# Performance work log

Measured on AMD Instinct MI355X. Metric: run time of the kernel, lower is better.

Reference implementation:

```python
import jax, jax.numpy as jnp
import numpy as np

DIM = 512
NUM_HEADS = 8
HEAD_SIZE = 64
INNER = NUM_HEADS * HEAD_SIZE  # 512


def setup_inputs() -> dict:
    key = jax.random.key(0)
    k1, k2, k3, k4, k5 = jax.random.split(key, 5)
    x = jax.random.normal(k1, (2, 4096, DIM), dtype=jnp.float32)
    # Linear params stored as [in, out] for y = x @ W + b (same math as torch Linear)
    w_qkv = jax.random.normal(k2, (DIM, INNER * 3), dtype=jnp.float32) * (1.0 / np.sqrt(DIM))
    b_qkv = jax.random.normal(k3, (INNER * 3,), dtype=jnp.float32) * 0.01
    w_out = jax.random.normal(k4, (INNER, DIM), dtype=jnp.float32) * (1.0 / np.sqrt(INNER))
    b_out = jax.random.normal(k5, (DIM,), dtype=jnp.float32) * 0.01
    return {"x": x, "w_qkv": w_qkv, "b_qkv": b_qkv, "w_out": w_out, "b_out": b_out}


def reference(x, w_qkv, b_qkv, w_out, b_out):
    b, n, _ = x.shape
    qkv = x @ w_qkv + b_qkv                      # [b, n, 3*inner]
    q, k, v = jnp.split(qkv, 3, axis=-1)          # each [b, n, inner]

    def heads(t):  # 'b n (h d) -> b h n d'
        return t.reshape(b, n, NUM_HEADS, HEAD_SIZE).transpose(0, 2, 1, 3)

    q, k, v = heads(q), heads(k), heads(v)
    scores = jnp.einsum('bhnd,bhmd->bhnm', q, k) / jnp.sqrt(jnp.float32(HEAD_SIZE))
    probs = jax.nn.softmax(scores, axis=-1)       # dropout is identity in eval
    out = jnp.einsum('bhnm,bhmd->bhnd', probs, v)
    out = out.transpose(0, 2, 1, 3).reshape(b, n, INNER)  # 'b h n d -> b n (h d)'
    return out @ w_out + b_out
```

## Files before the change

kernel.cpp:

```cpp
#include <hip/hip_runtime.h>

typedef __bf16 bf16;
typedef __bf16 bf16x8 __attribute__((ext_vector_type(8)));
typedef float f32x4 __attribute__((ext_vector_type(4)));
typedef unsigned u32x4 __attribute__((ext_vector_type(4)));

#define MFMA16(a, b, c) __builtin_amdgcn_mfma_f32_16x16x32_bf16((a), (b), (c), 0, 0, 0)

static __device__ __forceinline__ bf16x8 ldg8(const bf16* p) {
  return *(const bf16x8*)p;
}
static __device__ __forceinline__ unsigned cvt_pk_bf16(float lo, float hi) {
  unsigned d;
  asm("v_cvt_pk_bf16_f32 %0, %1, %2" : "=v"(d) : "v"(lo), "v"(hi));
  return d;
}
static __device__ __forceinline__ void pl32_swap(unsigned& a, unsigned& b) {
  asm("v_permlane32_swap_b32 %0, %1" : "+v"(a), "+v"(b));
}
static __device__ __forceinline__ void pl16_swap(unsigned& a, unsigned& b) {
  asm("v_permlane16_swap_b32 %0, %1" : "+v"(a), "+v"(b));
}


__global__ __launch_bounds__(256) void prep(const float* __restrict__ Wqkv,
                                            const float* __restrict__ Wout,
                                            const float* __restrict__ x,
                                            bf16* __restrict__ Wp1,
                                            bf16* __restrict__ Wp2,
                                            bf16* __restrict__ Xp) {
  __shared__ float tile[32 * 129];
  if (blockIdx.x < 16) {
    int kc = blockIdx.x, nt = blockIdx.y;
    const float* W;
    bf16* dst;
    int N, ntl;
    if (nt < 12) {
      W = Wqkv; N = 1536; ntl = nt;
      dst = Wp1 + ((size_t)ntl * 16 + kc) * 4096;
    } else {
      W = Wout; N = 512; ntl = nt - 12;
      dst = Wp2 + ((size_t)ntl * 16 + kc) * 4096;
    }
    int row = threadIdx.x >> 3;
    int c0 = (threadIdx.x & 7) * 16;
    const float* src = W + (size_t)(kc * 32 + row) * N + ntl * 128 + c0;
#pragma unroll
    for (int i = 0; i < 4; i++) {
      float4 v = *(const float4*)(src + i * 4);
      tile[row * 129 + c0 + i * 4 + 0] = v.x;
      tile[row * 129 + c0 + i * 4 + 1] = v.y;
      tile[row * 129 + c0 + i * 4 + 2] = v.z;
      tile[row * 129 + c0 + i * 4 + 3] = v.w;
    }
    __syncthreads();
#pragma unroll
    for (int half = 0; half < 2; half++) {
      int U = threadIdx.x + half * 256;
      int kchunk = U >> 7, n = U & 127;
      bf16x8 o;
#pragma unroll
      for (int j = 0; j < 8; j++) o[j] = (bf16)tile[(kchunk * 8 + j) * 129 + n];
      *(bf16x8*)&dst[U * 8] = o;
    }
  } else {
    int mt = blockIdx.x - 16, kc = blockIdx.y;
    int r = threadIdx.x >> 1;
    int khalf = threadIdx.x & 1;
    const float* src = x + (size_t)(mt * 128 + r) * 512 + kc * 32 + khalf * 16;
    float4 v0 = *(const float4*)(src + 0);
    float4 v1 = *(const float4*)(src + 4);
    float4 v2 = *(const float4*)(src + 8);
    float4 v3 = *(const float4*)(src + 12);
    bf16* dt = Xp + ((size_t)mt * 16 + kc) * 4096;
    bf16x8 a, b;
    a[0] = (bf16)v0.x; a[1] = (bf16)v0.y; a[2] = (bf16)v0.z; a[3] = (bf16)v0.w;
    a[4] = (bf16)v1.x; a[5] = (bf16)v1.y; a[6] = (bf16)v1.z; a[7] = (bf16)v1.w;
    b[0] = (bf16)v2.x; b[1] = (bf16)v2.y; b[2] = (bf16)v2.z; b[3] = (bf16)v2.w;
    b[4] = (bf16)v3.x; b[5] = (bf16)v3.y; b[6] = (bf16)v3.z; b[7] = (bf16)v3.w;
    int kc0 = khalf * 2;
    *(bf16x8*)&dt[(kc0 + 0) * 1024 + r * 8] = a;
    *(bf16x8*)&dt[(kc0 + 1) * 1024 + r * 8] = b;
  }
}

__global__ __launch_bounds__(256, 3) void qkv_gemm(const bf16* __restrict__ Xp,
                                                   const bf16* __restrict__ Wp1,
                                                   const float* __restrict__ bqkv,
                                                   bf16* __restrict__ Q,
                                                   bf16* __restrict__ Kh,
                                                   bf16* __restrict__ Vt) {
  int mt = blockIdx.x, nt = blockIdx.y;
  int tid = threadIdx.x;
  int wave = tid >> 6, lane = tid & 63;
  int l16 = lane & 15, quad = lane >> 4;
  int wr = wave >> 1, wc = wave & 1;

  __shared__ __align__(16) bf16 SM[9216];

  const bf16* At = Xp + (size_t)mt * 16 * 4096;
  const bf16* Bt = Wp1 + (size_t)nt * 16 * 4096;

  bf16x8 pa0 = ldg8(At + tid * 8);
  bf16x8 pa1 = ldg8(At + 2048 + tid * 8);

  f32x4 acc[4][4] = {};
#pragma unroll 2
  for (int kc = 0; kc < 16; kc++) {
    bf16* A = SM + (kc & 1) * 4096;
    *(bf16x8*)&A[tid * 8] = pa0;
    *(bf16x8*)&A[2048 + tid * 8] = pa1;
    __syncthreads();
    if (kc < 15) {
      const bf16* an = At + (kc + 1) * 4096;
      pa0 = ldg8(an + tid * 8);
      pa1 = ldg8(an + 2048 + tid * 8);
    }
    bf16x8 af[4], bfr[4];
#pragma unroll
    for (int fi = 0; fi < 4; fi++)
      af[fi] = *(const bf16x8*)&A[(quad * 128 + wr * 64 + fi * 16 + l16) * 8];
    const bf16* Bk = Bt + kc * 4096;
#pragma unroll
    for (int fj = 0; fj < 4; fj++)
      bfr[fj] = ldg8(Bk + (quad * 128 + wc * 64 + fj * 16 + l16) * 8);
    __builtin_amdgcn_s_setprio(1);
#pragma unroll
    for (int fi = 0; fi < 4; fi++)
#pragma unroll
      for (int fj = 0; fj < 4; fj++)
        acc[fi][fj] = MFMA16(af[fi], bfr[fj], acc[fi][fj]);
    __builtin_amdgcn_s_setprio(0);
  }

  __syncthreads();
  const int TS = 72;
  int b = mt >> 5;

  if (nt < 8) {
    bool isQ = nt < 4;
    bf16* dstb = isQ ? Q : Kh;
    int hb = isQ ? nt * 2 : (nt - 4) * 2;
#pragma unroll
    for (int ph = 0; ph < 2; ph++) {
      if (wc == ph) {
#pragma unroll
        for (int fj = 0; fj < 4; fj++) {
          float bias = bqkv[nt * 128 + wc * 64 + fj * 16 + l16];
#pragma unroll
          for (int fi = 0; fi < 4; fi++)
#pragma unroll
            for (int rr = 0; rr < 4; rr++) {
              float v = acc[fi][fj][rr] + bias;
              if (isQ) v *= 0.18033688f;
              SM[(wr * 64 + fi * 16 + quad * 4 + rr) * TS + fj * 16 + l16] =
                  (bf16)v;
            }
        }
      }
      __syncthreads();
      int bh = b * 8 + hb + ph;
      bf16* dh = dstb + (size_t)bh * 4096 * 64 + (size_t)((mt & 31) * 128) * 64;
#pragma unroll
      for (int i = 0; i < 4; i++) {
        int U = tid + i * 256;
        int mr = U >> 3, oct = U & 7;
        bf16x8 v = ldg8(&SM[mr * TS + oct * 8]);
        *(bf16x8*)&dh[(size_t)mr * 64 + oct * 8] = v;
      }
      __syncthreads();
    }
  } else {
    int h0 = (nt - 8) * 2;
#pragma unroll
    for (int ph = 0; ph < 2; ph++) {
      if (wr == ph) {
#pragma unroll
        for (int fj = 0; fj < 4; fj++) {
          float bias = bqkv[nt * 128 + wc * 64 + fj * 16 + l16];
          int cp = wc * 64 + fj * 16 + l16;
#pragma unroll
          for (int fi = 0; fi < 4; fi++)
#pragma unroll
            for (int rr = 0; rr < 4; rr++)
              SM[cp * TS + fi * 16 + quad * 4 + rr] =
                  (bf16)(acc[fi][fj][rr] + bias);
        }
      }
      __syncthreads();
      int nb = (mt & 31) * 2 + ph;
#pragma unroll
      for (int i = 0; i < 4; i++) {
        int U = tid + i * 256;
        int cp = U >> 3, oct = U & 7;
        int h = h0 + (cp >> 6), d = cp & 63;
        int bh = b * 8 + h;
        bf16x8 v = ldg8(&SM[cp * TS + oct * 8]);
        *(bf16x8*)&Vt[(((size_t)bh * 64 + nb) * 64 + d) * 64 + oct * 8] = v;
      }
      __syncthreads();
    }
  }
}

__global__ __launch_bounds__(256, 4) void flash_partial(const bf16* __restrict__ Q,
                                                        const bf16* __restrict__ K,
                                                        const bf16* __restrict__ Vt,
                                                        bf16* __restrict__ Opart,
                                                        float* __restrict__ Lpart) {
  int i = blockIdx.x;
  int swz = (i & 7) * 128 + (i >> 3);
  int half = swz & 1;
  int strip = (swz >> 1) & 31;
  int bh = swz >> 6;
  int tid = threadIdx.x;
  int wave = tid >> 6, lane = tid & 63;
  int l16 = lane & 15, quad = lane >> 4;

  const bf16* Qh = Q + (size_t)bh * 4096 * 64;
  const bf16* Kg = K + ((size_t)bh * 4096 + half * 2048) * 64;
  const bf16* Vg = Vt + (size_t)bh * 64 * 4096 + (size_t)half * 2048 * 64;

  __shared__ __align__(16) bf16 Klds[2][4096];
  __shared__ __align__(16) bf16 Vlds[2][4096];

  int qbase = strip * 128 + wave * 32;
  bf16x8 aq[2][2];
#pragma unroll
  for (int mt = 0; mt < 2; mt++) {
    const bf16* qr = Qh + (size_t)(qbase + mt * 16 + l16) * 64;
    aq[mt][0] = ldg8(qr + quad * 8);
    aq[mt][1] = ldg8(qr + 32 + quad * 8);
  }

  bf16x8 ones;
#pragma unroll
  for (int j = 0; j < 8; j++) ones[j] = (bf16)1.0f;

  f32x4 o[2][4] = {};
  f32x4 acc_l[2] = {};

  int e0 = tid * 8, e1 = (256 + tid) * 8;
  int r0 = e0 >> 6, r1 = e1 >> 6;
  int u0 = r0 * 8 + (((e0 & 63) >> 3) ^ (r0 & 7));
  int u1 = r1 * 8 + (((e1 & 63) >> 3) ^ (r1 & 7));

  bf16x8 kp0 = ldg8(Kg + e0), kp1 = ldg8(Kg + e1);
  bf16x8 vp0 = ldg8(Vg + e0), vp1 = ldg8(Vg + e1);

#pragma unroll 2
  for (int t = 0; t < 32; t++) {
    int cur = t & 1;
    bf16* kl = Klds[cur];
    bf16* vl = Vlds[cur];
    *(bf16x8*)&kl[u0 * 8] = kp0;
    *(bf16x8*)&kl[u1 * 8] = kp1;
    *(bf16x8*)&vl[u0 * 8] = vp0;
    *(bf16x8*)&vl[u1 * 8] = vp1;
    __syncthreads();

    if (t < 31) {
      const bf16* kg = Kg + (size_t)(t + 1) * 4096;
      const bf16* vg = Vg + (size_t)(t + 1) * 4096;
      kp0 = ldg8(kg + e0);
      kp1 = ldg8(kg + e1);
      vp0 = ldg8(vg + e0);
      vp1 = ldg8(vg + e1);
    }

#pragma unroll
    for (int h2 = 0; h2 < 2; h2++) {
      f32x4 s[2][2] = {};
      __builtin_amdgcn_s_setprio(1);
#pragma unroll
      for (int c2 = 0; c2 < 2; c2++) {
        int n = h2 * 32 + c2 * 16 + l16;
        bf16x8 k0 = *(const bf16x8*)&kl[(n * 8 + (quad ^ (n & 7))) * 8];
        bf16x8 k1 = *(const bf16x8*)&kl[(n * 8 + ((4 + quad) ^ (n & 7))) * 8];
#pragma unroll
        for (int mt = 0; mt < 2; mt++) {
          s[mt][c2] = MFMA16(k0, aq[mt][0], s[mt][c2]);
          s[mt][c2] = MFMA16(k1, aq[mt][1], s[mt][c2]);
        }
      }
      __builtin_amdgcn_s_setprio(0);

      bf16x8 pa[2];
#pragma unroll
      for (int mt = 0; mt < 2; mt++) {
        unsigned ue[2], wo[2];
#pragma unroll
        for (int c2 = 0; c2 < 2; c2++) {
          float p0 = __builtin_amdgcn_exp2f(s[mt][c2][0]);
          float p1 = __builtin_amdgcn_exp2f(s[mt][c2][1]);
          float p2 = __builtin_amdgcn_exp2f(s[mt][c2][2]);
          float p3 = __builtin_amdgcn_exp2f(s[mt][c2][3]);
          ue[c2] = cvt_pk_bf16(p0, p1);
          wo[c2] = cvt_pk_bf16(p2, p3);
        }
        pl32_swap(ue[0], ue[1]);
        pl16_swap(ue[0], ue[1]);
        pl32_swap(wo[0], wo[1]);
        pl16_swap(wo[0], wo[1]);
        u32x4 pk = {ue[0], wo[0], ue[1], wo[1]};
        pa[mt] = __builtin_bit_cast(bf16x8, pk);
      }

      __builtin_amdgcn_s_setprio(1);
      acc_l[0] = MFMA16(pa[0], ones, acc_l[0]);
      acc_l[1] = MFMA16(pa[1], ones, acc_l[1]);
#pragma unroll
      for (int ct = 0; ct < 4; ct++) {
        int d = ct * 16 + l16;
        bf16x8 bv = *(const bf16x8*)&vl[(d * 8 + ((h2 * 4 + quad) ^ (d & 7))) * 8];
        o[0][ct] = MFMA16(pa[0], bv, o[0][ct]);
        o[1][ct] = MFMA16(pa[1], bv, o[1][ct]);
      }
      __builtin_amdgcn_s_setprio(0);
    }
  }

  size_t ub = ((size_t)half * 16 + bh) * 32 + strip;
  bf16* op = Opart + ub * 8192;
#pragma unroll
  for (int mt = 0; mt < 2; mt++) {
#pragma unroll
    for (int ct = 0; ct < 4; ct++)
#pragma unroll
      for (int r = 0; r < 4; r++)
        op[(wave * 32 + mt * 16 + quad * 4 + r) * 64 + ct * 16 + l16] =
            (bf16)o[mt][ct][r];
    if (l16 == 0) {
#pragma unroll
      for (int r = 0; r < 4; r++)
        Lpart[ub * 128 + wave * 32 + mt * 16 + quad * 4 + r] = acc_l[mt][r];
    }
  }
}

__global__ __launch_bounds__(256, 4) void out_gemm(const bf16* __restrict__ Opart,
                                                   const float* __restrict__ Lpart,
                                                   const bf16* __restrict__ Wp2,
                                                   const float* __restrict__ bout,
                                                   float* __restrict__ Out) {
  int mt = blockIdx.x, nt = blockIdx.y;
  int tid = threadIdx.x;
  int wave = tid >> 6, lane = tid & 63;
  int l16 = lane & 15, quad = lane >> 4;
  int mt128 = mt >> 1, mhalf = mt & 1;
  int b = mt128 >> 5, strip = mt128 & 31;
  int r = mhalf * 64 + lane;

  __shared__ __align__(16) bf16 SM[2][2048];

  const bf16* Bt = Wp2 + (size_t)nt * 16 * 4096;

  bf16x8 po0, po1;
  float pls;
  {
    int h = 0, d0 = 0;
    int bh = b * 8 + h;
    size_t s0 = ((size_t)bh * 32 + strip);
    size_t s1 = (((size_t)16 + bh) * 32 + strip);
    po0 = ldg8(&Opart[s0 * 8192 + r * 64 + d0 + wave * 8]);
    po1 = ldg8(&Opart[s1 * 8192 + r * 64 + d0 + wave * 8]);
    pls = Lpart[s0 * 128 + r] + Lpart[s1 * 128 + r];
  }

  f32x4 acc[4][2] = {};
#pragma unroll 2
  for (int kc = 0; kc < 16; kc++) {
    bf16* A = SM[kc & 1];
    float rl = 1.0f / pls;
    u32x4 pk = {
        cvt_pk_bf16(((float)po0[0] + (float)po1[0]) * rl,
                    ((float)po0[1] + (float)po1[1]) * rl),
        cvt_pk_bf16(((float)po0[2] + (float)po1[2]) * rl,
                    ((float)po0[3] + (float)po1[3]) * rl),
        cvt_pk_bf16(((float)po0[4] + (float)po1[4]) * rl,
                    ((float)po0[5] + (float)po1[5]) * rl),
        cvt_pk_bf16(((float)po0[6] + (float)po1[6]) * rl,
                    ((float)po0[7] + (float)po1[7]) * rl)};
    *(bf16x8*)&A[tid * 8] = __builtin_bit_cast(bf16x8, pk);
    __syncthreads();
    if (kc < 15) {
      int kn = kc + 1;
      int h = kn >> 1, d0 = (kn & 1) * 32;
      int bh = b * 8 + h;
      size_t s0 = ((size_t)bh * 32 + strip);
      size_t s1 = (((size_t)16 + bh) * 32 + strip);
      po0 = ldg8(&Opart[s0 * 8192 + r * 64 + d0 + wave * 8]);
      po1 = ldg8(&Opart[s1 * 8192 + r * 64 + d0 + wave * 8]);
      pls = Lpart[s0 * 128 + r] + Lpart[s1 * 128 + r];
    }
    bf16x8 af[4], bfr[2];
#pragma unroll
    for (int fi = 0; fi < 4; fi++)
      af[fi] = *(const bf16x8*)&A[(quad * 64 + fi * 16 + l16) * 8];
    const bf16* Bk = Bt + kc * 4096;
#pragma unroll
    for (int fj = 0; fj < 2; fj++)
      bfr[fj] = ldg8(Bk + (quad * 128 + wave * 32 + fj * 16 + l16) * 8);
    __builtin_amdgcn_s_setprio(1);
#pragma unroll
    for (int fi = 0; fi < 4; fi++)
#pragma unroll
      for (int fj = 0; fj < 2; fj++)
        acc[fi][fj] = MFMA16(af[fi], bfr[fj], acc[fi][fj]);
    __builtin_amdgcn_s_setprio(0);
  }

#pragma unroll
  for (int fj = 0; fj < 2; fj++) {
    int c = nt * 128 + wave * 32 + fj * 16 + l16;
    float bias = bout[c];
#pragma unroll
    for (int fi = 0; fi < 4; fi++) {
#pragma unroll
      for (int rr = 0; rr < 4; rr++) {
        int m = mt * 64 + fi * 16 + quad * 4 + rr;
        Out[(size_t)m * 512 + c] = acc[fi][fj][rr] + bias;
      }
    }
  }
}

extern "C" void kernel_launch(void* const* d_in, const int* in_sizes, int n_in,
                              void* d_out, int out_size, void* d_ws,
                              size_t ws_size, hipStream_t stream) {
  const float* x = (const float*)d_in[0];
  const float* w_qkv = (const float*)d_in[1];
  const float* b_qkv = (const float*)d_in[2];
  const float* w_out = (const float*)d_in[3];
  const float* b_out = (const float*)d_in[4];
  float* out = (float*)d_out;

  char* ws = (char*)d_ws;
  bf16* Q = (bf16*)(ws + 0);
  bf16* K = (bf16*)(ws + 8388608);
  bf16* Vt = (bf16*)(ws + 16777216);
  bf16* Wp2 = (bf16*)(ws + 25165824);
  bf16* Opart = (bf16*)(ws + 25690112);
  float* Lpart = (float*)(ws + 42467328);
  bf16* Wp1 = (bf16*)(ws + 42991616);
  bf16* Xp = (bf16*)(ws + 44564480);

  prep<<<dim3(80, 16), 256, 0, stream>>>(w_qkv, w_out, x, Wp1, Wp2, Xp);
  qkv_gemm<<<dim3(64, 12), 256, 0, stream>>>(Xp, Wp1, b_qkv, Q, K, Vt);
  flash_partial<<<dim3(1024), 256, 0, stream>>>(Q, K, Vt, Opart, Lpart);
  out_gemm<<<dim3(128, 4), 256, 0, stream>>>(Opart, Lpart, Wp2, b_out, out);
}
```

Baseline: 191.7 us.

## Split flash attention KV range into quarters for more blocks and occupancy

The flash partial kernel now splits each head's key/value range into four quarters instead of two, launching twice as many blocks with 32-key tiles and half the shared memory, and raises the launch bound to 8 blocks per CU. The output GEMM is updated to sum four partial outputs and normalisers, and the workspace is reorganised so Opart overlaps the prep buffers, which are dead by then. The aim is better occupancy and load balance in attention. The cost is extra partial-output traffic and a heavier reduction in the output GEMM.

New measurement: 766.2 us. +299.8%, slower.

```diff
diff --git a/kernel.cpp b/kernel.cpp
--- a/kernel.cpp
+++ b/kernel.cpp
@@ -203,26 +203,26 @@
   }
 }
 
-__global__ __launch_bounds__(256, 4) void flash_partial(const bf16* __restrict__ Q,
+__global__ __launch_bounds__(256, 8) void flash_partial(const bf16* __restrict__ Q,
                                                         const bf16* __restrict__ K,
                                                         const bf16* __restrict__ Vt,
                                                         bf16* __restrict__ Opart,
                                                         float* __restrict__ Lpart) {
   int i = blockIdx.x;
-  int swz = (i & 7) * 128 + (i >> 3);
-  int half = swz & 1;
-  int strip = (swz >> 1) & 31;
-  int bh = swz >> 6;
+  int swz = (i & 7) * 256 + (i >> 3);
+  int qtr = swz & 3;
+  int strip = (swz >> 2) & 31;
+  int bh = swz >> 7;
   int tid = threadIdx.x;
   int wave = tid >> 6, lane = tid & 63;
   int l16 = lane & 15, quad = lane >> 4;
 
   const bf16* Qh = Q + (size_t)bh * 4096 * 64;
-  const bf16* Kg = K + ((size_t)bh * 4096 + half * 2048) * 64;
-  const bf16* Vg = Vt + (size_t)bh * 64 * 4096 + (size_t)half * 2048 * 64;
-
-  __shared__ __align__(16) bf16 Klds[2][4096];
-  __shared__ __align__(16) bf16 Vlds[2][4096];
+  const bf16* Kg = K + ((size_t)bh * 4096 + qtr * 1024) * 64;
+  const bf16* Vg = Vt + (size_t)bh * 64 * 4096 + (size_t)qtr * 1024 * 64;
+
+  __shared__ __align__(16) bf16 Klds[2][2048];
+  __shared__ __align__(16) bf16 Vlds[2][2048];
 
   int qbase = strip * 128 + wave * 32;
   bf16x8 aq[2][2];
@@ -240,87 +240,77 @@
   f32x4 o[2][4] = {};
   f32x4 acc_l[2] = {};
 
-  int e0 = tid * 8, e1 = (256 + tid) * 8;
-  int r0 = e0 >> 6, r1 = e1 >> 6;
-  int u0 = r0 * 8 + (((e0 & 63) >> 3) ^ (r0 & 7));
-  int u1 = r1 * 8 + (((e1 & 63) >> 3) ^ (r1 & 7));
-
-  bf16x8 kp0 = ldg8(Kg + e0), kp1 = ldg8(Kg + e1);
-  bf16x8 vp0 = ldg8(Vg + e0), vp1 = ldg8(Vg + e1);
+  int ku = (tid >> 3) * 8 + ((tid & 7) ^ ((tid >> 3) & 7));
+  int vd = tid >> 2, vc8 = (tid & 3) * 8;
+  int vu = vd * 4 + ((tid & 3) ^ ((vd >> 1) & 3));
+
+  bf16x8 kp = ldg8(Kg + tid * 8);
+  bf16x8 vp = ldg8(Vg + (size_t)vd * 64 + vc8);
 
 #pragma unroll 2
   for (int t = 0; t < 32; t++) {
-    int cur = t & 1;
-    bf16* kl = Klds[cur];
-    bf16* vl = Vlds[cur];
-    *(bf16x8*)&kl[u0 * 8] = kp0;
-    *(bf16x8*)&kl[u1 * 8] = kp1;
-    *(bf16x8*)&vl[u0 * 8] = vp0;
-    *(bf16x8*)&vl[u1 * 8] = vp1;
+    bf16* kl = Klds[t & 1];
+    bf16* vl = Vlds[t & 1];
+    *(bf16x8*)&kl[ku * 8] = kp;
+    *(bf16x8*)&vl[vu * 8] = vp;
     __syncthreads();
 
     if (t < 31) {
-      const bf16* kg = Kg + (size_t)(t + 1) * 4096;
-      const bf16* vg = Vg + (size_t)(t + 1) * 4096;
-      kp0 = ldg8(kg + e0);
-      kp1 = ldg8(kg + e1);
-      vp0 = ldg8(vg + e0);
-      vp1 = ldg8(vg + e1);
-    }
-
-#pragma unroll
-    for (int h2 = 0; h2 < 2; h2++) {
-      f32x4 s[2][2] = {};
-      __builtin_amdgcn_s_setprio(1);
+      kp = ldg8(Kg + (size_t)(t + 1) * 2048 + tid * 8);
+      vp = ldg8(Vg + (size_t)((t + 1) >> 1) * 4096 + ((t + 1) & 1) * 32 +
+                (size_t)vd * 64 + vc8);
+    }
+
+    f32x4 s[2][2] = {};
+    __builtin_amdgcn_s_setprio(1);
+#pragma unroll
+    for (int c2 = 0; c2 < 2; c2++) {
+      int n = c2 * 16 + l16;
+      bf16x8 k0 = *(const bf16x8*)&kl[(n * 8 + (quad ^ (n & 7))) * 8];
+      bf16x8 k1 = *(const bf16x8*)&kl[(n * 8 + ((4 + quad) ^ (n & 7))) * 8];
+#pragma unroll
+      for (int mt = 0; mt < 2; mt++) {
+        s[mt][c2] = MFMA16(k0, aq[mt][0], s[mt][c2]);
+        s[mt][c2] = MFMA16(k1, aq[mt][1], s[mt][c2]);
+      }
+    }
+    __builtin_amdgcn_s_setprio(0);
+
+    bf16x8 pa[2];
+#pragma unroll
+    for (int mt = 0; mt < 2; mt++) {
+      unsigned ue[2], wo[2];
 #pragma unroll
       for (int c2 = 0; c2 < 2; c2++) {
-        int n = h2 * 32 + c2 * 16 + l16;
-        bf16x8 k0 = *(const bf16x8*)&kl[(n * 8 + (quad ^ (n & 7))) * 8];
-        bf16x8 k1 = *(const bf16x8*)&kl[(n * 8 + ((4 + quad) ^ (n & 7))) * 8];
-#pragma unroll
-        for (int mt = 0; mt < 2; mt++) {
-          s[mt][c2] = MFMA16(k0, aq[mt][0], s[mt][c2]);
-          s[mt][c2] = MFMA16(k1, aq[mt][1], s[mt][c2]);
-        }
-      }
-      __builtin_amdgcn_s_setprio(0);
-
-      bf16x8 pa[2];
-#pragma unroll
-      for (int mt = 0; mt < 2; mt++) {
-        unsigned ue[2], wo[2];
-#pragma unroll
-        for (int c2 = 0; c2 < 2; c2++) {
-          float p0 = __builtin_amdgcn_exp2f(s[mt][c2][0]);
-          float p1 = __builtin_amdgcn_exp2f(s[mt][c2][1]);
-          float p2 = __builtin_amdgcn_exp2f(s[mt][c2][2]);
-          float p3 = __builtin_amdgcn_exp2f(s[mt][c2][3]);
-          ue[c2] = cvt_pk_bf16(p0, p1);
-          wo[c2] = cvt_pk_bf16(p2, p3);
-        }
-        pl32_swap(ue[0], ue[1]);
-        pl16_swap(ue[0], ue[1]);
-        pl32_swap(wo[0], wo[1]);
-        pl16_swap(wo[0], wo[1]);
-        u32x4 pk = {ue[0], wo[0], ue[1], wo[1]};
-        pa[mt] = __builtin_bit_cast(bf16x8, pk);
-      }
-
-      __builtin_amdgcn_s_setprio(1);
-      acc_l[0] = MFMA16(pa[0], ones, acc_l[0]);
-      acc_l[1] = MFMA16(pa[1], ones, acc_l[1]);
-#pragma unroll
-      for (int ct = 0; ct < 4; ct++) {
-        int d = ct * 16 + l16;
-        bf16x8 bv = *(const bf16x8*)&vl[(d * 8 + ((h2 * 4 + quad) ^ (d & 7))) * 8];
-        o[0][ct] = MFMA16(pa[0], bv, o[0][ct]);
-        o[1][ct] = MFMA16(pa[1], bv, o[1][ct]);
-      }
-      __builtin_amdgcn_s_setprio(0);
-    }
-  }
-
-  size_t ub = ((size_t)half * 16 + bh) * 32 + strip;
+        float p0 = __builtin_amdgcn_exp2f(s[mt][c2][0]);
+        float p1 = __builtin_amdgcn_exp2f(s[mt][c2][1]);
+        float p2 = __builtin_amdgcn_exp2f(s[mt][c2][2]);
+        float p3 = __builtin_amdgcn_exp2f(s[mt][c2][3]);
+        ue[c2] = cvt_pk_bf16(p0, p1);
+        wo[c2] = cvt_pk_bf16(p2, p3);
+      }
+      pl32_swap(ue[0], ue[1]);
+      pl16_swap(ue[0], ue[1]);
+      pl32_swap(wo[0], wo[1]);
+      pl16_swap(wo[0], wo[1]);
+      u32x4 pk = {ue[0], wo[0], ue[1], wo[1]};
+      pa[mt] = __builtin_bit_cast(bf16x8, pk);
+    }
+
+    __builtin_amdgcn_s_setprio(1);
+    acc_l[0] = MFMA16(pa[0], ones, acc_l[0]);
+    acc_l[1] = MFMA16(pa[1], ones, acc_l[1]);
+#pragma unroll
+    for (int ct = 0; ct < 4; ct++) {
+      int d = ct * 16 + l16;
+      bf16x8 bv = *(const bf16x8*)&vl[(d * 4 + (quad ^ ((d >> 1) & 3))) * 8];
+      o[0][ct] = MFMA16(pa[0], bv, o[0][ct]);
+      o[1][ct] = MFMA16(pa[1], bv, o[1][ct]);
+    }
+    __builtin_amdgcn_s_setprio(0);
+  }
+
+  size_t ub = ((size_t)qtr * 16 + bh) * 32 + strip;
   bf16* op = Opart + ub * 8192;
 #pragma unroll
   for (int mt = 0; mt < 2; mt++) {
@@ -355,16 +345,17 @@
 
   const bf16* Bt = Wp2 + (size_t)nt * 16 * 4096;
 
-  bf16x8 po0, po1;
+  bf16x8 po[4];
   float pls;
   {
-    int h = 0, d0 = 0;
-    int bh = b * 8 + h;
-    size_t s0 = ((size_t)bh * 32 + strip);
-    size_t s1 = (((size_t)16 + bh) * 32 + strip);
-    po0 = ldg8(&Opart[s0 * 8192 + r * 64 + d0 + wave * 8]);
-    po1 = ldg8(&Opart[s1 * 8192 + r * 64 + d0 + wave * 8]);
-    pls = Lpart[s0 * 128 + r] + Lpart[s1 * 128 + r];
+    int bh = b * 8;
+    pls = 0.f;
+#pragma unroll
+    for (int q = 0; q < 4; q++) {
+      size_t u = ((size_t)q * 16 + bh) * 32 + strip;
+      po[q] = ldg8(&Opart[u * 8192 + r * 64 + wave * 8]);
+      pls += Lpart[u * 128 + r];
+    }
   }
 
   f32x4 acc[4][2] = {};
@@ -372,26 +363,26 @@
   for (int kc = 0; kc < 16; kc++) {
     bf16* A = SM[kc & 1];
     float rl = 1.0f / pls;
-    u32x4 pk = {
-        cvt_pk_bf16(((float)po0[0] + (float)po1[0]) * rl,
-                    ((float)po0[1] + (float)po1[1]) * rl),
-        cvt_pk_bf16(((float)po0[2] + (float)po1[2]) * rl,
-                    ((float)po0[3] + (float)po1[3]) * rl),
-        cvt_pk_bf16(((float)po0[4] + (float)po1[4]) * rl,
-                    ((float)po0[5] + (float)po1[5]) * rl),
-        cvt_pk_bf16(((float)po0[6] + (float)po1[6]) * rl,
-                    ((float)po0[7] + (float)po1[7]) * rl)};
+    float sj[8];
+#pragma unroll
+    for (int j = 0; j < 8; j++)
+      sj[j] = (((float)po[0][j] + (float)po[1][j]) +
+               ((float)po[2][j] + (float)po[3][j])) * rl;
+    u32x4 pk = {cvt_pk_bf16(sj[0], sj[1]), cvt_pk_bf16(sj[2], sj[3]),
+                cvt_pk_bf16(sj[4], sj[5]), cvt_pk_bf16(sj[6], sj[7])};
     *(bf16x8*)&A[tid * 8] = __builtin_bit_cast(bf16x8, pk);
     __syncthreads();
     if (kc < 15) {
       int kn = kc + 1;
       int h = kn >> 1, d0 = (kn & 1) * 32;
       int bh = b * 8 + h;
-      size_t s0 = ((size_t)bh * 32 + strip);
-      size_t s1 = (((size_t)16 + bh) * 32 + strip);
-      po0 = ldg8(&Opart[s0 * 8192 + r * 64 + d0 + wave * 8]);
-      po1 = ldg8(&Opart[s1 * 8192 + r * 64 + d0 + wave * 8]);
-      pls = Lpart[s0 * 128 + r] + Lpart[s1 * 128 + r];
+      pls = 0.f;
+#pragma unroll
+      for (int q = 0; q < 4; q++) {
+        size_t u = ((size_t)q * 16 + bh) * 32 + strip;
+        po[q] = ldg8(&Opart[u * 8192 + r * 64 + d0 + wave * 8]);
+        pls += Lpart[u * 128 + r];
+      }
     }
     bf16x8 af[4], bfr[2];
 #pragma unroll
@@ -441,12 +432,12 @@
   bf16* Vt = (bf16*)(ws + 16777216);
   bf16* Wp2 = (bf16*)(ws + 25165824);
   bf16* Opart = (bf16*)(ws + 25690112);
-  float* Lpart = (float*)(ws + 42467328);
-  bf16* Wp1 = (bf16*)(ws + 42991616);
-  bf16* Xp = (bf16*)(ws + 44564480);
+  float* Lpart = (float*)(ws + 59244544);
+  bf16* Xp = (bf16*)(ws + 25690112);
+  bf16* Wp1 = (bf16*)(ws + 34078720);
 
   prep<<<dim3(80, 16), 256, 0, stream>>>(w_qkv, w_out, x, Wp1, Wp2, Xp);
   qkv_gemm<<<dim3(64, 12), 256, 0, stream>>>(Xp, Wp1, b_qkv, Q, K, Vt);
-  flash_partial<<<dim3(1024), 256, 0, stream>>>(Q, K, Vt, Opart, Lpart);
+  flash_partial<<<dim3(2048), 256, 0, stream>>>(Q, K, Vt, Opart, Lpart);
   out_gemm<<<dim3(128, 4), 256, 0, stream>>>(Opart, Lpart, Wp2, b_out, out);
 }
```
